# Optimization experiments

Hardware: AMD Instinct MI355X
Metric: run time of the kernel (lower is better)

Reference implementation:

```python
import jax, jax.numpy as jnp
import numpy as np
from jax import lax

EPS = 1e-5
N_WIRES, N_LAYERS = 4, 3
DIM = 2 ** N_WIRES  # 16

# Static CNOT permutations for control w, target w+1 (state @ CNOT => new[k] = old[k ^ (((k>>c)&1)<<t)])
_idx = np.arange(DIM)
CNOT_PERMS = [jnp.asarray(_idx ^ (((_idx >> w) & 1) << (w + 1))) for w in range(N_WIRES - 1)]


def conv3x3(x, w):
    # x: [B,1,H,W], w: [1,1,3,3], padding=1, no bias
    return lax.conv_general_dilated(x, w, (1, 1), 'SAME',
                                    dimension_numbers=('NCHW', 'OIHW', 'NCHW'))


def batchnorm_train(x, gamma, beta):
    # training-mode BN: batch statistics over (B,H,W), biased variance
    mean = jnp.mean(x, axis=(0, 2, 3), keepdims=True)
    var = jnp.var(x, axis=(0, 2, 3), keepdims=True)
    xn = (x - mean) * lax.rsqrt(var + EPS)
    return xn * gamma.reshape(1, -1, 1, 1) + beta.reshape(1, -1, 1, 1)


def residual_block(x, w1, g1, b1, w2, g2, b2):
    out = jax.nn.relu(batchnorm_train(conv3x3(x, w1), g1, b1))
    out = batchnorm_train(conv3x3(out, w2), g2, b2)
    return jax.nn.relu(out + x)


def quantum_feat4(theta):
    # Faithful to QuantumKernel: real state, each RZ scales by cos(theta/2)
    # (rz[0,0]==rz[1,1]==cos(theta/2)), CNOT is a bit-indexed permutation.
    # State is independent of the patch values (patch is never used).
    s = jnp.zeros(DIM, dtype=theta.dtype).at[0].set(1.0)
    for l in range(N_LAYERS):
        s = s * jnp.prod(jnp.cos(theta[l] / 2.0))  # 8 RZ scalings for this layer
        for w in range(N_WIRES - 1):
            s = s[CNOT_PERMS[w]]
    probs = s ** 2
    return probs[:4]


def setup_inputs() -> dict:
    key = jax.random.key(0)
    ks = jax.random.split(key, 12)
    B = 16384
    d = dict(
        x=jax.random.normal(ks[0], (B, 1, 28, 28), dtype=jnp.float32),
        theta=jax.random.normal(ks[1], (N_LAYERS, N_WIRES, 2), dtype=jnp.float32),
        r1_w1=jax.random.normal(ks[2], (1, 1, 3, 3), dtype=jnp.float32) * 0.3,
        r1_g1=jnp.ones((1,), jnp.float32), r1_b1=jnp.zeros((1,), jnp.float32),
        r1_w2=jax.random.normal(ks[3], (1, 1, 3, 3), dtype=jnp.float32) * 0.3,
        r1_g2=jnp.ones((1,), jnp.float32), r1_b2=jnp.zeros((1,), jnp.float32),
        r2_w1=jax.random.normal(ks[4], (1, 1, 3, 3), dtype=jnp.float32) * 0.3,
        r2_g1=jnp.ones((1,), jnp.float32), r2_b1=jnp.zeros((1,), jnp.float32),
        r2_w2=jax.random.normal(ks[5], (1, 1, 3, 3), dtype=jnp.float32) * 0.3,
        r2_g2=jnp.ones((1,), jnp.float32), r2_b2=jnp.zeros((1,), jnp.float32),
        fc_w=jax.random.normal(ks[6], (10, 784), dtype=jnp.float32) * 0.03,
        fc_b=jnp.zeros((10,), jnp.float32),
        alpha=jnp.asarray(0.5, dtype=jnp.float32),
    )
    return d


def reference(x, theta, r1_w1, r1_g1, r1_b1, r1_w2, r1_g2, r1_b2,
              r2_w1, r2_g1, r2_b1, r2_w2, r2_g2, r2_b2, fc_w, fc_b, alpha):
    B = x.shape[0]
    cls_feat = residual_block(x, r1_w1, r1_g1, r1_b1, r1_w2, r1_g2, r1_b2)
    cls_feat = residual_block(cls_feat, r2_w1, r2_g1, r2_b1, r2_w2, r2_g2, r2_b2)
    cls_flat = cls_feat.reshape(B, -1)  # [B, 784]

    # Quantum filter: kernel output ignores patch values, identical for all
    # 196 patches and all batch elements; cat along dim=1 -> tile the 4-vector.
    p4 = quantum_feat4(theta)                           # [4]
    q_feat = jnp.broadcast_to(jnp.tile(p4, 14 * 14), (B, 784))

    fused = alpha * cls_flat + (1.0 - alpha) * q_feat
    logits = fused @ fc_w.T + fc_b
    return jax.nn.log_softmax(logits, axis=-1)
```

## Files before the change

kernel.cpp:

```cpp
#include <hip/hip_runtime.h>
#include <hip/hip_fp16.h>
#include <math.h>

#define BATCH   16384
#define IMGPIX  784
#define NTOT    (BATCH * IMGPIX)
#define NSLOT   64
#define SLOTSTR 8
#define STAGE_DBL (NSLOT * SLOTSTR)
#define TROW 224
#define TGRP 6272
#define CONVBLK 3584

struct __align__(8) h4 { __half2 lo, hi; };
__device__ __forceinline__ h4 f4_to_h4(float4 v) {
    h4 r; r.lo = __floats2half2_rn(v.x, v.y); r.hi = __floats2half2_rn(v.z, v.w); return r;
}
__device__ __forceinline__ float4 h4_to_f4(h4 p) {
    float2 a = __half22float2(p.lo), b = __half22float2(p.hi);
    return make_float4(a.x, a.y, b.x, b.y);
}
#define ZERO4 make_float4(0.f, 0.f, 0.f, 0.f)

__device__ __forceinline__ void wave_stats_atomic(double lsum, double lsq, double* slot) {
    #pragma unroll
    for (int off = 32; off >= 1; off >>= 1) {
        lsum += __shfl_down(lsum, off, 64);
        lsq  += __shfl_down(lsq,  off, 64);
    }
    if ((threadIdx.x & 63) == 0) {
        atomicAdd(&slot[0], lsum);
        atomicAdd(&slot[1], lsq);
    }
}

__device__ __forceinline__ float2 stats_ab(const double* __restrict__ stats_in,
                                           float gamma, float beta) {
    int lane = threadIdx.x & 63;
    double s = stats_in[lane * SLOTSTR];
    double q = stats_in[lane * SLOTSTR + 1];
    #pragma unroll
    for (int off = 32; off >= 1; off >>= 1) {
        s += __shfl_down(s, off, 64);
        q += __shfl_down(q, off, 64);
    }
    s = __shfl(s, 0, 64);
    q = __shfl(q, 0, 64);
    const double INV_N = 1.0 / (double)NTOT;
    double mean = s * INV_N;
    double var  = q * INV_N - mean * mean;
    float rstd = 1.0f / sqrtf((float)var + 1e-5f);
    float a  = gamma * rstd;
    float bb = beta - (float)mean * a;
    return make_float2(a, bb);
}

__device__ __forceinline__ float4 hrow(float wl, float wc, float wr,
                                       float L, float4 v, float R) {
    float4 h;
    h.x = fmaf(wl, L,   fmaf(wc, v.x, wr * v.y));
    h.y = fmaf(wl, v.x, fmaf(wc, v.y, wr * v.z));
    h.z = fmaf(wl, v.y, fmaf(wc, v.z, wr * v.w));
    h.w = fmaf(wl, v.z, fmaf(wc, v.w, wr * R));
    return h;
}

__device__ __forceinline__ void emit_row(__half* dst, int r, float4 o, float mf,
                                         double& lsum, double& lsq, bool act) {
    if (act) *(h4*)(dst + r * TROW) = f4_to_h4(o);
    float s4 = (o.x + o.y) + (o.z + o.w);
    float q4 = fmaf(o.x, o.x, fmaf(o.y, o.y, fmaf(o.z, o.z, o.w * o.w)));
    lsum += (double)(mf * s4);
    lsq  += (double)(mf * q4);
}

#define LANE_SETUP()                                                          \
    const int t = threadIdx.x;                                                \
    const int lane = t & 63;                                                  \
    const int widx = t >> 6;                                                  \
    const int c4   = lane & 7;                                                \
    const bool act = (c4 < 7);                                                \
    const float mf = act ? 1.f : 0.f;                                         \
    const int c4c  = c4 < 7 ? c4 : 6;                                         \
    const int task = blockIdx.x * 4 + widx;                     \
    const int s    = task >> 11;                              \
    const int G    = task & 2047;                          \
    const int r0   = s * 4;                                                   \
    const int rtop = (r0 > 0)  ? (r0 - 1) : 0;                                \
    const int rbot = (r0 < 24) ? (r0 + 4) : 27;                               \
    const int i8   = lane >> 3;                                               \
    const int img  = G * 8 + i8;                                              \
    const size_t xbase = (size_t)img * IMGPIX + c4c * 4;                      \
    const size_t tbR   = (size_t)G * TGRP + c4c * 32 + i8 * 4;                \
    const size_t tbW   = (size_t)G * TGRP + c4  * 32 + i8 * 4;

#define CONV_STEP(k, v)                                                       \
    {                                                                         \
        float L = __shfl_up((v).w, 1, 64);  if (c4 == 0) L = 0.f;             \
        float R = __shfl_down((v).x, 1, 64); if (c4 == 6) R = 0.f;            \
        float4 h2 = hrow(w9[6], w9[7], w9[8], L, (v), R);                     \
        float4 h1 = hrow(w9[3], w9[4], w9[5], L, (v), R);                     \
        float4 h0 = hrow(w9[0], w9[1], w9[2], L, (v), R);                     \
        accA.x += h2.x; accA.y += h2.y; accA.z += h2.z; accA.w += h2.w;       \
        if ((k) >= 2) emit_row(dst, r0 + (k) - 2, accA, mf, lsum, lsq, act);  \
        accA.x = accB.x + h1.x; accA.y = accB.y + h1.y;                       \
        accA.z = accB.z + h1.z; accA.w = accB.w + h1.w;                       \
        accB = h0;                                                            \
    }

#define HALO_ZERO(k, v)                                                       \
    if ((k) == 0 && r0 == 0)  (v) = ZERO4;                                    \
    if ((k) == 5 && r0 == 24) (v) = ZERO4;

__global__ __launch_bounds__(256, 8) void k_conv_plain(const float* __restrict__ in,
        const float* __restrict__ w, __half* __restrict__ out,
        __half* __restrict__ x16_out, double* __restrict__ stats_out)
{
    LANE_SETUP();
    float w9[9];
    #pragma unroll
    for (int i = 0; i < 9; i++) w9[i] = w[i];
    const float* src = in + xbase;
    __half* dst  = out + tbW;
    __half* dstx = x16_out + tbW;

    float4 vb[6];
    vb[0] = *(const float4*)(src + rtop * 28);
    #pragma unroll
    for (int k = 1; k < 5; k++) vb[k] = *(const float4*)(src + (r0 - 1 + k) * 28);
    vb[5] = *(const float4*)(src + rbot * 28);
    __builtin_amdgcn_sched_barrier(0);

    float4 accA = ZERO4, accB = ZERO4;
    double lsum = 0.0, lsq = 0.0;
    #pragma unroll
    for (int k = 0; k < 6; k++) {
        float4 v = vb[k];
        if (act && k >= 1 && k <= 4)
            *(h4*)(dstx + (r0 - 1 + k) * TROW) = f4_to_h4(vb[k]);
        HALO_ZERO(k, v);
        CONV_STEP(k, v);
    }
    wave_stats_atomic(lsum, lsq, &stats_out[(task & (NSLOT - 1)) * SLOTSTR]);
}

__global__ __launch_bounds__(256, 8) void k_conv_affine(const __half* __restrict__ in,
        const double* __restrict__ stats_in,
        const float* __restrict__ gamma, const float* __restrict__ beta,
        const float* __restrict__ w, __half* __restrict__ out, double* __restrict__ stats_out)
{
    LANE_SETUP();
    float2 ab = stats_ab(stats_in, gamma[0], beta[0]);
    float w9[9];
    #pragma unroll
    for (int i = 0; i < 9; i++) w9[i] = w[i];
    const __half* src = in + tbR;
    __half* dst = out + tbW;

    h4 vb[6];
    vb[0] = *(const h4*)(src + rtop * TROW);
    #pragma unroll
    for (int k = 1; k < 5; k++) vb[k] = *(const h4*)(src + (r0 - 1 + k) * TROW);
    vb[5] = *(const h4*)(src + rbot * TROW);
    __builtin_amdgcn_sched_barrier(0);

    float4 accA = ZERO4, accB = ZERO4;
    double lsum = 0.0, lsq = 0.0;
    #pragma unroll
    for (int k = 0; k < 6; k++) {
        float4 r4 = h4_to_f4(vb[k]);
        float4 v;
        v.x = fmaxf(fmaf(ab.x, r4.x, ab.y), 0.f);
        v.y = fmaxf(fmaf(ab.x, r4.y, ab.y), 0.f);
        v.z = fmaxf(fmaf(ab.x, r4.z, ab.y), 0.f);
        v.w = fmaxf(fmaf(ab.x, r4.w, ab.y), 0.f);
        HALO_ZERO(k, v);
        CONV_STEP(k, v);
    }
    wave_stats_atomic(lsum, lsq, &stats_out[(task & (NSLOT - 1)) * SLOTSTR]);
}

__global__ __launch_bounds__(256, 8) void k_conv_resid(const __half* __restrict__ y2,
        const __half* __restrict__ x16, const double* __restrict__ stats_in,
        const float* __restrict__ gamma, const float* __restrict__ beta,
        const float* __restrict__ w, __half* __restrict__ y3_out,
        __half* __restrict__ o1_out, double* __restrict__ stats_out)
{
    LANE_SETUP();
    float2 ab = stats_ab(stats_in, gamma[0], beta[0]);
    float w9[9];
    #pragma unroll
    for (int i = 0; i < 9; i++) w9[i] = w[i];
    const __half* srcy = y2 + tbR;
    const __half* srcx = x16 + tbR;
    __half* dst  = y3_out + tbW;
    __half* dsto = o1_out + tbW;

    h4 yb[6], xb[6];
    yb[0] = *(const h4*)(srcy + rtop * TROW);
    xb[0] = *(const h4*)(srcx + rtop * TROW);
    #pragma unroll
    for (int k = 1; k < 5; k++) {
        yb[k] = *(const h4*)(srcy + (r0 - 1 + k) * TROW);
        xb[k] = *(const h4*)(srcx + (r0 - 1 + k) * TROW);
    }
    yb[5] = *(const h4*)(srcy + rbot * TROW);
    xb[5] = *(const h4*)(srcx + rbot * TROW);
    __builtin_amdgcn_sched_barrier(0);

    float4 accA = ZERO4, accB = ZERO4;
    double lsum = 0.0, lsq = 0.0;
    #pragma unroll
    for (int k = 0; k < 6; k++) {
        float4 r4 = h4_to_f4(yb[k]);
        float4 x4 = h4_to_f4(xb[k]);
        float4 v;
        v.x = fmaxf(fmaf(ab.x, r4.x, ab.y) + x4.x, 0.f);
        v.y = fmaxf(fmaf(ab.x, r4.y, ab.y) + x4.y, 0.f);
        v.z = fmaxf(fmaf(ab.x, r4.z, ab.y) + x4.z, 0.f);
        v.w = fmaxf(fmaf(ab.x, r4.w, ab.y) + x4.w, 0.f);
        HALO_ZERO(k, v);
        if (act && k >= 1 && k <= 4)
            *(h4*)(dsto + (r0 - 1 + k) * TROW) = f4_to_h4(v);
        CONV_STEP(k, v);
    }
    wave_stats_atomic(lsum, lsq, &stats_out[(task & (NSLOT - 1)) * SLOTSTR]);
}

__global__ __launch_bounds__(256) void k_head(const __half* __restrict__ y4,
        const __half* __restrict__ o1, const double* __restrict__ stats_in,
        const float* __restrict__ gamma, const float* __restrict__ beta,
        const float* __restrict__ fc_w, const float* __restrict__ qk,
        const float* __restrict__ alpha_p, float* __restrict__ out)
{
    __shared__ float fcK[7840];
    const int t = threadIdx.x;
    float2 ab = stats_ab(stats_in, gamma[0], beta[0]);
    for (int idx = t; idx < 7840; idx += 256) fcK[idx] = fc_w[idx];
    float alpha = alpha_p[0];
    float qkr[10];
    #pragma unroll
    for (int k = 0; k < 10; k++) qkr[k] = qk[k];
    __syncthreads();

    const int lane = t & 63;
    const int widx = t >> 6;
    const int c4   = lane & 7;
    const int i8   = lane >> 3;
    const int c4c  = c4 < 7 ? c4 : 6;
    const float mf = (c4 < 7) ? 1.f : 0.f;
    const int G    = blockIdx.x * 4 + widx;
    const size_t tb = (size_t)G * TGRP + c4c * 32 + i8 * 4;
    const __half* ya = y4 + tb;
    const __half* oa = o1 + tb;

    float acc[10];
    #pragma unroll
    for (int k = 0; k < 10; k++) acc[k] = 0.f;

    #pragma unroll 7
    for (int r = 0; r < 28; r++) {
        float4 yf = h4_to_f4(*(const h4*)(ya + r * TROW));
        float4 of = h4_to_f4(*(const h4*)(oa + r * TROW));
        float4 v;
        v.x = fmaxf(fmaf(ab.x, yf.x, ab.y) + of.x, 0.f);
        v.y = fmaxf(fmaf(ab.x, yf.y, ab.y) + of.y, 0.f);
        v.z = fmaxf(fmaf(ab.x, yf.z, ab.y) + of.z, 0.f);
        v.w = fmaxf(fmaf(ab.x, yf.w, ab.y) + of.w, 0.f);
        const float* fb = &fcK[r * 28 + c4c * 4];
        #pragma unroll
        for (int k = 0; k < 10; k++) {
            const float4 f = *(const float4*)(fb + k * 784);
            acc[k] = fmaf(v.x, f.x, fmaf(v.y, f.y, fmaf(v.z, f.z, fmaf(v.w, f.w, acc[k]))));
        }
    }
    #pragma unroll
    for (int k = 0; k < 10; k++) {
        acc[k] *= mf;
        acc[k] += __shfl_xor(acc[k], 1, 64);
        acc[k] += __shfl_xor(acc[k], 2, 64);
        acc[k] += __shfl_xor(acc[k], 4, 64);
    }
    float l[10];
    float m = -1e30f;
    #pragma unroll
    for (int k = 0; k < 10; k++) {
        l[k] = fmaf(alpha, acc[k], qkr[k]);
        m = fmaxf(m, l[k]);
    }
    float se = 0.f;
    #pragma unroll
    for (int k = 0; k < 10; k++) se += __expf(l[k] - m);
    float lse = m + __logf(se);
    if (c4 == 0) {
        int img = G * 8 + i8;
        #pragma unroll
        for (int k = 0; k < 10; k++) out[(size_t)img * 10 + k] = l[k] - lse;
    }
}

__global__ __launch_bounds__(256) void k_init(const float* __restrict__ theta,
        const float* __restrict__ fc_w, const float* __restrict__ fc_b,
        const float* __restrict__ alpha_p, float* __restrict__ qk, double* __restrict__ stats)
{
    const int t = threadIdx.x;
    for (int i = t; i < 4 * STAGE_DBL; i += 256) stats[i] = 0.0;
    __shared__ float csum[10];
    if (t < 80) {
        int k = t >> 3, oct = t & 7;
        float s = 0.f;
        #pragma unroll
        for (int i = 0; i < 25; i++) {
            int p = oct + 8 * i;
            if (p < 196) s += fc_w[k * 784 + p * 4];
        }
        s += __shfl_xor(s, 1, 64);
        s += __shfl_xor(s, 2, 64);
        s += __shfl_xor(s, 4, 64);
        if (oct == 0) csum[k] = s;
    }
    __syncthreads();
    if (t < 10) {
        float c = 1.f;
        #pragma unroll
        for (int i = 0; i < 24; i++) c *= cosf(theta[i] * 0.5f);
        float c2 = c * c;
        qk[t] = (1.f - alpha_p[0]) * c2 * csum[t] + fc_b[t];
    }
}

extern "C" void kernel_launch(void* const* d_in, const int* in_sizes, int n_in,
                              void* d_out, int out_size, void* d_ws, size_t ws_size,
                              hipStream_t stream) {
    const float* x     = (const float*)d_in[0];
    const float* theta = (const float*)d_in[1];
    const float* r1_w1 = (const float*)d_in[2];
    const float* r1_g1 = (const float*)d_in[3];
    const float* r1_b1 = (const float*)d_in[4];
    const float* r1_w2 = (const float*)d_in[5];
    const float* r1_g2 = (const float*)d_in[6];
    const float* r1_b2 = (const float*)d_in[7];
    const float* r2_w1 = (const float*)d_in[8];
    const float* r2_g1 = (const float*)d_in[9];
    const float* r2_b1 = (const float*)d_in[10];
    const float* r2_w2 = (const float*)d_in[11];
    const float* r2_g2 = (const float*)d_in[12];
    const float* r2_b2 = (const float*)d_in[13];
    const float* fc_w  = (const float*)d_in[14];
    const float* fc_b  = (const float*)d_in[15];
    const float* alpha = (const float*)d_in[16];
    float* out = (float*)d_out;

    double* stats = (double*)d_ws;
    float*  qk    = (float*)((char*)d_ws + 16384);
    __half* bufA  = (__half*)((char*)d_ws + 32768);
    __half* bufB  = bufA + (size_t)NTOT;
    __half* bufD  = bufB + (size_t)NTOT;
    __half* bufX  = bufD + (size_t)NTOT;

    double* s_y1 = stats + 0 * STAGE_DBL;
    double* s_y2 = stats + 1 * STAGE_DBL;
    double* s_y3 = stats + 2 * STAGE_DBL;
    double* s_y4 = stats + 3 * STAGE_DBL;

    k_init<<<1, 256, 0, stream>>>(theta, fc_w, fc_b, alpha, qk, stats);
    k_conv_plain<<<CONVBLK, 256, 0, stream>>>(x, r1_w1, bufA, bufX, s_y1);
    k_conv_affine<<<CONVBLK, 256, 0, stream>>>(bufA, s_y1, r1_g1, r1_b1, r1_w2, bufB, s_y2);
    k_conv_resid<<<CONVBLK, 256, 0, stream>>>(bufB, bufX, s_y2, r1_g2, r1_b2, r2_w1, bufA, bufD, s_y3);
    k_conv_affine<<<CONVBLK, 256, 0, stream>>>(bufA, s_y3, r2_g1, r2_b1, r2_w2, bufB, s_y4);
    k_head<<<512, 256, 0, stream>>>(bufB, bufD, s_y4, r2_g2, r2_b2, fc_w, qk, alpha, out);
}
```

Before: 108.1 us.

## Recompute first conv in second stage instead of storing it; fold init into head

The first conv kernel now only computes batch statistics and stores the fp16 input copy. It no longer writes its conv output. A new fused kernel reloads the fp16 input with a 2-row halo, recomputes conv1 into registers, applies BN+ReLU and runs conv2. This trades one full fp16 write and read of an activation buffer for redundant conv arithmetic and higher register pressure (launch bounds reduced to 6 waves). The init kernel is replaced by a memset, and the quantum/fc-bias constant is computed inside the head kernel, which removes one launch.

```diff
diff --git a/kernel.cpp b/kernel.cpp
--- a/kernel.cpp
+++ b/kernel.cpp
@@ -94,18 +94,44 @@
     const size_t tbR   = (size_t)G * TGRP + c4c * 32 + i8 * 4;                \
     const size_t tbW   = (size_t)G * TGRP + c4  * 32 + i8 * 4;
 
-#define CONV_STEP(k, v)                                                       \
-    {                                                                         \
+#define CSTEP_CORE(WW, v)                                                     \
         float L = __shfl_up((v).w, 1, 64);  if (c4 == 0) L = 0.f;             \
         float R = __shfl_down((v).x, 1, 64); if (c4 == 6) R = 0.f;            \
-        float4 h2 = hrow(w9[6], w9[7], w9[8], L, (v), R);                     \
-        float4 h1 = hrow(w9[3], w9[4], w9[5], L, (v), R);                     \
-        float4 h0 = hrow(w9[0], w9[1], w9[2], L, (v), R);                     \
-        accA.x += h2.x; accA.y += h2.y; accA.z += h2.z; accA.w += h2.w;       \
-        if ((k) >= 2) emit_row(dst, r0 + (k) - 2, accA, mf, lsum, lsq, act);  \
+        float4 h2 = hrow(WW[6], WW[7], WW[8], L, (v), R);                     \
+        float4 h1 = hrow(WW[3], WW[4], WW[5], L, (v), R);                     \
+        float4 h0 = hrow(WW[0], WW[1], WW[2], L, (v), R);                     \
+        accA.x += h2.x; accA.y += h2.y; accA.z += h2.z; accA.w += h2.w;
+
+#define CSTEP_TAIL()                                                          \
         accA.x = accB.x + h1.x; accA.y = accB.y + h1.y;                       \
         accA.z = accB.z + h1.z; accA.w = accB.w + h1.w;                       \
-        accB = h0;                                                            \
+        accB = h0;
+
+#define CSTEP_OUT(WW, k, v)                                                   \
+    {                                                                         \
+        CSTEP_CORE(WW, v)                                                     \
+        if ((k) >= 2) emit_row(dst, r0 + (k) - 2, accA, mf, lsum, lsq, act);  \
+        CSTEP_TAIL()                                                          \
+    }
+
+#define CSTEP_STATS(WW, k, v)                                                 \
+    {                                                                         \
+        CSTEP_CORE(WW, v)                                                     \
+        if ((k) >= 2) {                                                       \
+            float s4 = (accA.x + accA.y) + (accA.z + accA.w);                 \
+            float q4 = fmaf(accA.x, accA.x, fmaf(accA.y, accA.y,              \
+                       fmaf(accA.z, accA.z, accA.w * accA.w)));               \
+            lsum += (double)(mf * s4);                                        \
+            lsq  += (double)(mf * q4);                                        \
+        }                                                                     \
+        CSTEP_TAIL()                                                          \
+    }
+
+#define CSTEP_REG(WW, j, v)                                                   \
+    {                                                                         \
+        CSTEP_CORE(WW, v)                                                     \
+        if ((j) >= 2) hbuf[(j) - 2] = accA;                                   \
+        CSTEP_TAIL()                                                          \
     }
 
 #define HALO_ZERO(k, v)                                                       \
@@ -113,15 +139,14 @@
     if ((k) == 5 && r0 == 24) (v) = ZERO4;
 
 __global__ __launch_bounds__(256, 8) void k_conv_plain(const float* __restrict__ in,
-        const float* __restrict__ w, __half* __restrict__ out,
-        __half* __restrict__ x16_out, double* __restrict__ stats_out)
+        const float* __restrict__ w, __half* __restrict__ x16_out,
+        double* __restrict__ stats_out)
 {
     LANE_SETUP();
     float w9[9];
     #pragma unroll
     for (int i = 0; i < 9; i++) w9[i] = w[i];
     const float* src = in + xbase;
-    __half* dst  = out + tbW;
     __half* dstx = x16_out + tbW;
 
     float4 vb[6];
@@ -139,7 +164,56 @@
         if (act && k >= 1 && k <= 4)
             *(h4*)(dstx + (r0 - 1 + k) * TROW) = f4_to_h4(vb[k]);
         HALO_ZERO(k, v);
-        CONV_STEP(k, v);
+        CSTEP_STATS(w9, k, v);
+    }
+    wave_stats_atomic(lsum, lsq, &stats_out[(task & (NSLOT - 1)) * SLOTSTR]);
+}
+
+__global__ __launch_bounds__(256, 6) void k_conv_affine_rc(
+        const __half* __restrict__ x16, const double* __restrict__ stats_in,
+        const float* __restrict__ gamma, const float* __restrict__ beta,
+        const float* __restrict__ wc1, const float* __restrict__ wc2,
+        __half* __restrict__ out, double* __restrict__ stats_out)
+{
+    LANE_SETUP();
+    float2 ab = stats_ab(stats_in, gamma[0], beta[0]);
+    float wA[9], wB[9];
+    #pragma unroll
+    for (int i = 0; i < 9; i++) { wA[i] = wc1[i]; wB[i] = wc2[i]; }
+    const __half* src = x16 + tbR;
+    __half* dst = out + tbW;
+
+    h4 xb[8];
+    #pragma unroll
+    for (int j = 0; j < 8; j++) {
+        int rr = r0 - 2 + j;
+        int rc = rr < 0 ? 0 : (rr > 27 ? 27 : rr);
+        xb[j] = *(const h4*)(src + rc * TROW);
+    }
+    __builtin_amdgcn_sched_barrier(0);
+
+    float4 hbuf[6];
+    float4 accA = ZERO4, accB = ZERO4;
+    #pragma unroll
+    for (int j = 0; j < 8; j++) {
+        float4 v = h4_to_f4(xb[j]);
+        int rr = r0 - 2 + j;
+        if (rr < 0 || rr > 27) v = ZERO4;
+        CSTEP_REG(wA, j, v);
+    }
+
+    accA = ZERO4; accB = ZERO4;
+    double lsum = 0.0, lsq = 0.0;
+    #pragma unroll
+    for (int k = 0; k < 6; k++) {
+        float4 r4 = hbuf[k];
+        float4 v;
+        v.x = fmaxf(fmaf(ab.x, r4.x, ab.y), 0.f);
+        v.y = fmaxf(fmaf(ab.x, r4.y, ab.y), 0.f);
+        v.z = fmaxf(fmaf(ab.x, r4.z, ab.y), 0.f);
+        v.w = fmaxf(fmaf(ab.x, r4.w, ab.y), 0.f);
+        HALO_ZERO(k, v);
+        CSTEP_OUT(wB, k, v);
     }
     wave_stats_atomic(lsum, lsq, &stats_out[(task & (NSLOT - 1)) * SLOTSTR]);
 }
@@ -175,7 +249,7 @@
         v.z = fmaxf(fmaf(ab.x, r4.z, ab.y), 0.f);
         v.w = fmaxf(fmaf(ab.x, r4.w, ab.y), 0.f);
         HALO_ZERO(k, v);
-        CONV_STEP(k, v);
+        CSTEP_OUT(w9, k, v);
     }
     wave_stats_atomic(lsum, lsq, &stats_out[(task & (NSLOT - 1)) * SLOTSTR]);
 }
@@ -222,7 +296,7 @@
         HALO_ZERO(k, v);
         if (act && k >= 1 && k <= 4)
             *(h4*)(dsto + (r0 - 1 + k) * TROW) = f4_to_h4(v);
-        CONV_STEP(k, v);
+        CSTEP_OUT(w9, k, v);
     }
     wave_stats_atomic(lsum, lsq, &stats_out[(task & (NSLOT - 1)) * SLOTSTR]);
 }
@@ -230,18 +304,39 @@
 __global__ __launch_bounds__(256) void k_head(const __half* __restrict__ y4,
         const __half* __restrict__ o1, const double* __restrict__ stats_in,
         const float* __restrict__ gamma, const float* __restrict__ beta,
-        const float* __restrict__ fc_w, const float* __restrict__ qk,
-        const float* __restrict__ alpha_p, float* __restrict__ out)
+        const float* __restrict__ fc_w, const float* __restrict__ fc_b,
+        const float* __restrict__ theta, const float* __restrict__ alpha_p,
+        float* __restrict__ out)
 {
     __shared__ float fcK[7840];
+    __shared__ float qk_s[10];
     const int t = threadIdx.x;
     float2 ab = stats_ab(stats_in, gamma[0], beta[0]);
     for (int idx = t; idx < 7840; idx += 256) fcK[idx] = fc_w[idx];
+    __syncthreads();
+    if (t < 80) {
+        int k = t >> 3, oct = t & 7;
+        float s = 0.f;
+        #pragma unroll
+        for (int i = 0; i < 25; i++) {
+            int p = oct + 8 * i;
+            if (p < 196) s += fcK[k * 784 + p * 4];
+        }
+        s += __shfl_xor(s, 1, 64);
+        s += __shfl_xor(s, 2, 64);
+        s += __shfl_xor(s, 4, 64);
+        if (oct == 0) qk_s[k] = s;
+    }
+    __syncthreads();
+
     float alpha = alpha_p[0];
+    float c = 1.f;
+    #pragma unroll
+    for (int i = 0; i < 24; i++) c *= cosf(theta[i] * 0.5f);
+    float c2s = (1.f - alpha) * c * c;
     float qkr[10];
     #pragma unroll
-    for (int k = 0; k < 10; k++) qkr[k] = qk[k];
-    __syncthreads();
+    for (int k = 0; k < 10; k++) qkr[k] = fmaf(c2s, qk_s[k], fc_b[k]);
 
     const int lane = t & 63;
     const int widx = t >> 6;
@@ -296,36 +391,6 @@
         int img = G * 8 + i8;
         #pragma unroll
         for (int k = 0; k < 10; k++) out[(size_t)img * 10 + k] = l[k] - lse;
-    }
-}
-
-__global__ __launch_bounds__(256) void k_init(const float* __restrict__ theta,
-        const float* __restrict__ fc_w, const float* __restrict__ fc_b,
-        const float* __restrict__ alpha_p, float* __restrict__ qk, double* __restrict__ stats)
-{
-    const int t = threadIdx.x;
-    for (int i = t; i < 4 * STAGE_DBL; i += 256) stats[i] = 0.0;
-    __shared__ float csum[10];
-    if (t < 80) {
-        int k = t >> 3, oct = t & 7;
-        float s = 0.f;
-        #pragma unroll
-        for (int i = 0; i < 25; i++) {
-            int p = oct + 8 * i;
-            if (p < 196) s += fc_w[k * 784 + p * 4];
-        }
-        s += __shfl_xor(s, 1, 64);
-        s += __shfl_xor(s, 2, 64);
-        s += __shfl_xor(s, 4, 64);
-        if (oct == 0) csum[k] = s;
-    }
-    __syncthreads();
-    if (t < 10) {
-        float c = 1.f;
-        #pragma unroll
-        for (int i = 0; i < 24; i++) c *= cosf(theta[i] * 0.5f);
-        float c2 = c * c;
-        qk[t] = (1.f - alpha_p[0]) * c2 * csum[t] + fc_b[t];
     }
 }
 
@@ -352,7 +417,6 @@
     float* out = (float*)d_out;
 
     double* stats = (double*)d_ws;
-    float*  qk    = (float*)((char*)d_ws + 16384);
     __half* bufA  = (__half*)((char*)d_ws + 32768);
     __half* bufB  = bufA + (size_t)NTOT;
     __half* bufD  = bufB + (size_t)NTOT;
@@ -363,10 +427,14 @@
     double* s_y3 = stats + 2 * STAGE_DBL;
     double* s_y4 = stats + 3 * STAGE_DBL;
 
-    k_init<<<1, 256, 0, stream>>>(theta, fc_w, fc_b, alpha, qk, stats);
-    k_conv_plain<<<CONVBLK, 256, 0, stream>>>(x, r1_w1, bufA, bufX, s_y1);
-    k_conv_affine<<<CONVBLK, 256, 0, stream>>>(bufA, s_y1, r1_g1, r1_b1, r1_w2, bufB, s_y2);
-    k_conv_resid<<<CONVBLK, 256, 0, stream>>>(bufB, bufX, s_y2, r1_g2, r1_b2, r2_w1, bufA, bufD, s_y3);
-    k_conv_affine<<<CONVBLK, 256, 0, stream>>>(bufA, s_y3, r2_g1, r2_b1, r2_w2, bufB, s_y4);
-    k_head<<<512, 256, 0, stream>>>(bufB, bufD, s_y4, r2_g2, r2_b2, fc_w, qk, alpha, out);
-}
+    hipMemsetAsync(stats, 0, 4 * STAGE_DBL * sizeof(double), stream);
+    k_conv_plain<<<CONVBLK, 256, 0, stream>>>(x, r1_w1, bufX, s_y1);
+    k_conv_affine_rc<<<CONVBLK, 256, 0, stream>>>(bufX, s_y1, r1_g1, r1_b1,
+                                                  r1_w1, r1_w2, bufB, s_y2);
+    k_conv_resid<<<CONVBLK, 256, 0, stream>>>(bufB, bufX, s_y2, r1_g2, r1_b2,
+                                              r2_w1, bufA, bufD, s_y3);
+    k_conv_affine<<<CONVBLK, 256, 0, stream>>>(bufA, s_y3, r2_g1, r2_b1,
+                                               r2_w2, bufB, s_y4);
+    k_head<<<512, 256, 0, stream>>>(bufB, bufD, s_y4, r2_g2, r2_b2,
+                                    fc_w, fc_b, theta, alpha, out);
+}
```

After: 113.0 us. 4.6% more time.
